# Kernel tuning notes

Measured on AMD Instinct MI355X. Metric: run time of the kernel, lower is better.

The kernel has to match this reference:

```python
import jax, jax.numpy as jnp
import numpy as np

N = 100000
E = 1600000
IN_FEATS = 256
HID = 128


def _graph_conv(x, W, b, src, dst, n_nodes):
    # DGL GraphConv with norm='both':
    #   out = D_in^{-1/2} * A * (D_out^{-1/2} * x @ W) + b
    ones = jnp.ones(src.shape[0], dtype=x.dtype)
    deg_out = jax.ops.segment_sum(ones, src, num_segments=n_nodes)
    deg_in = jax.ops.segment_sum(ones, dst, num_segments=n_nodes)
    norm_src = jnp.maximum(deg_out, 1.0) ** -0.5  # [N]
    norm_dst = jnp.maximum(deg_in, 1.0) ** -0.5   # [N]
    h = (x * norm_src[:, None]) @ W               # [N, HID]
    msg = h[src]                                  # [E, HID] gather
    agg = jax.ops.segment_sum(msg, dst, num_segments=n_nodes)  # [N, HID] scatter-add
    return agg * norm_dst[:, None] + b


def setup_inputs() -> dict:
    key = jax.random.key(0)
    ks = jax.random.split(key, 12)
    x = jax.random.normal(ks[0], (N, IN_FEATS), dtype=jnp.float32)
    src0 = jax.random.randint(ks[1], (E,), 0, N, dtype=jnp.int32)
    dst0 = jax.random.randint(ks[2], (E,), 0, N, dtype=jnp.int32)
    src1 = jax.random.randint(ks[3], (E,), 0, N, dtype=jnp.int32)
    dst1 = jax.random.randint(ks[4], (E,), 0, N, dtype=jnp.int32)
    s_e = 1.0 / np.sqrt(IN_FEATS)
    s_h = 1.0 / np.sqrt(HID)
    We = jax.random.uniform(ks[5], (IN_FEATS, HID), jnp.float32, -s_e, s_e)
    be = jax.random.uniform(ks[6], (HID,), jnp.float32, -s_e, s_e)
    W1 = jax.random.uniform(ks[7], (HID, HID), jnp.float32, -s_h, s_h)
    b1 = jnp.zeros((HID,), jnp.float32)
    W2 = jax.random.uniform(ks[8], (HID, HID), jnp.float32, -s_h, s_h)
    b2 = jnp.zeros((HID,), jnp.float32)
    return {"x": x, "We": We, "be": be, "W1": W1, "b1": b1, "W2": W2, "b2": b2,
            "src0": src0, "dst0": dst0, "src1": src1, "dst1": dst1}


def reference(x, We, be, W1, b1, W2, b2, src0, dst0, src1, dst1):
    n = x.shape[0]
    h = x @ We + be                                   # embed
    h = jax.nn.relu(_graph_conv(h, W1, b1, src0, dst0, n))
    h = jax.nn.relu(_graph_conv(h, W2, b2, src1, dst1, n))
    return h
```

## Files before the change

kernel.cpp:

```cpp
#include <hip/hip_runtime.h>

#define HID 128
#define NBUCK 512
#define BSHIFT 8
#define NB 512
#define M4 (4 * NBUCK * NB)
#define STAGE_CAP 8192

typedef __attribute__((ext_vector_type(8))) short bf16x8;
typedef __attribute__((ext_vector_type(4))) float f32x4;

__device__ __forceinline__ unsigned short f2bf(float f) {
    union { float f; unsigned u; } v; v.f = f;
    unsigned r = v.u + 0x7fff + ((v.u >> 16) & 1);
    return (unsigned short)(r >> 16);
}
__device__ __forceinline__ float bf2f(unsigned short b) {
    union { float f; unsigned u; } v; v.u = ((unsigned)b) << 16;
    return v.f;
}

__global__ __launch_bounds__(256) void bucket_count_all(
    const int* __restrict__ k0, const int* __restrict__ k1,
    const int* __restrict__ k2, const int* __restrict__ k3,
    int* __restrict__ counts, int E, int chunk) {
    __shared__ int h[4][NBUCK];
    int tid = threadIdx.x;
    #pragma unroll
    for (int j = 0; j < 8; ++j) ((int*)h)[tid + j * 256] = 0;
    __syncthreads();
    int base = blockIdx.x * chunk;
    int end = min(base + chunk, E);
    const int* keys[4] = {k0, k1, k2, k3};
    #pragma unroll
    for (int p = 0; p < 4; ++p) {
        const int* kp = keys[p];
        for (int i = base + tid; i < end; i += 256)
            atomicAdd(&h[p][kp[i] >> BSHIFT], 1);
    }
    __syncthreads();
    #pragma unroll
    for (int p = 0; p < 4; ++p) {
        counts[((p << 9) + tid) * NB + blockIdx.x] = h[p][tid];
        counts[((p << 9) + tid + 256) * NB + blockIdx.x] = h[p][tid + 256];
    }
}

__global__ __launch_bounds__(256) void scan_a(int* __restrict__ data, int* __restrict__ partials, int m) {
    __shared__ int sdata[256];
    int base = blockIdx.x * 1024;
    int tid = threadIdx.x;
    int v[4]; int s = 0;
    #pragma unroll
    for (int i = 0; i < 4; ++i) { int idx = base + tid * 4 + i; v[i] = (idx < m) ? data[idx] : 0; s += v[i]; }
    sdata[tid] = s; __syncthreads();
    for (int off = 1; off < 256; off <<= 1) {
        int t = (tid >= off) ? sdata[tid - off] : 0; __syncthreads();
        sdata[tid] += t; __syncthreads();
    }
    int excl = sdata[tid] - s;
    if (tid == 255) partials[blockIdx.x] = sdata[255];
    int run = excl;
    #pragma unroll
    for (int i = 0; i < 4; ++i) { int idx = base + tid * 4 + i; if (idx < m) data[idx] = run; run += v[i]; }
}

__global__ __launch_bounds__(1024) void scan_b(int* __restrict__ partials, int nb) {
    __shared__ int sdata[1024];
    int tid = threadIdx.x;
    int v = (tid < nb) ? partials[tid] : 0;
    sdata[tid] = v; __syncthreads();
    for (int off = 1; off < 1024; off <<= 1) {
        int t = (tid >= off) ? sdata[tid - off] : 0; __syncthreads();
        sdata[tid] += t; __syncthreads();
    }
    if (tid < nb) partials[tid] = sdata[tid] - v;
}

__global__ __launch_bounds__(256) void scan_c(int* __restrict__ data, const int* __restrict__ partials, int m) {
    int i = blockIdx.x * 256 + threadIdx.x;
    if (i < m) data[i] += partials[i >> 10];
}

__global__ __launch_bounds__(256) void bucket_scatter_all(
    const int* __restrict__ k0, const int* __restrict__ k1,
    const int* __restrict__ k2, const int* __restrict__ k3,
    const int* __restrict__ pay0, const int* __restrict__ pay1,
    const int* __restrict__ scanned, unsigned* __restrict__ bucketed,
    int E, int chunk) {
    __shared__ unsigned cur[4][NBUCK];
    int tid = threadIdx.x;
    int blk = blockIdx.x;
    #pragma unroll
    for (int p = 0; p < 4; ++p) {
        cur[p][tid]       = (unsigned)scanned[((p << 9) + tid) * NB + blk];
        cur[p][tid + 256] = (unsigned)scanned[((p << 9) + tid + 256) * NB + blk];
    }
    __syncthreads();
    int base = blk * chunk;
    int end = min(base + chunk, E);
    const int* keys[4] = {k0, k1, k2, k3};
    const int* pays[4] = {pay0, pay1, nullptr, nullptr};
    #pragma unroll
    for (int p = 0; p < 4; ++p) {
        const int* kp = keys[p];
        const int* pp = pays[p];
        for (int i = base + tid; i < end; i += 256) {
            int k = kp[i];
            int b = k >> BSHIFT;
            unsigned pay = pp ? (unsigned)pp[i] : 0u;
            unsigned pos = atomicAdd(&cur[p][b], 1u);
            bucketed[pos] = ((unsigned)(k & 255) << 17) | pay;
        }
    }
}

__global__ __launch_bounds__(256) void bucket_finalize(
    unsigned* __restrict__ bucketed, const int* __restrict__ scanned,
    int* __restrict__ rowptr0, int* __restrict__ rowptr1,
    int* __restrict__ dout0, int* __restrict__ dout1, int n, int E) {
    __shared__ unsigned stage[STAGE_CAP];
    __shared__ int cnt[256];
    __shared__ int sd[256];
    __shared__ int excl[256];
    __shared__ int cur[256];
    int tid = threadIdx.x;
    int g = blockIdx.x;
    int p = g >> 9;
    int b = g & 511;
    int start = scanned[g * NB];
    int end = (g == 4 * NBUCK - 1) ? 4 * E : scanned[(g + 1) * NB];
    if (end - start > STAGE_CAP) end = start + STAGE_CAP;
    int len = end - start;
    int node0 = b << BSHIFT;

    cnt[tid] = 0;
    __syncthreads();
    if (p < 2) {
        for (int i = tid; i < len; i += 256) {
            unsigned v = bucketed[start + i];
            stage[i] = v;
            atomicAdd(&cnt[v >> 17], 1);
        }
    } else {
        for (int i = tid; i < len; i += 256)
            atomicAdd(&cnt[bucketed[start + i] >> 17], 1);
    }
    __syncthreads();

    if (p >= 2) {
        int* dout = (p == 2) ? dout0 : dout1;
        int node = node0 + tid;
        if (node < n) dout[node] = cnt[tid];
        return;
    }

    int v = cnt[tid];
    sd[tid] = v;
    __syncthreads();
    for (int off = 1; off < 256; off <<= 1) {
        int t = (tid >= off) ? sd[tid - off] : 0; __syncthreads();
        sd[tid] += t; __syncthreads();
    }
    excl[tid] = sd[tid] - v;
    cur[tid] = 0;
    __syncthreads();

    int startLocal = start - p * E;
    int* rp = (p == 0) ? rowptr0 : rowptr1;
    int node = node0 + tid;
    if (node < n) rp[node] = startLocal + excl[tid];
    if (b == NBUCK - 1 && tid == 0) rp[n] = E;

    int* csr = (int*)bucketed + p * E;
    for (int i = tid; i < len; i += 256) {
        unsigned w = stage[i];
        int nl = (int)(w >> 17);
        int pos = startLocal + excl[nl] + atomicAdd(&cur[nl], 1);
        csr[pos] = (int)(w & 0x1FFFFu);
    }
}

__device__ __forceinline__ size_t bswz_idx(int k, int col) {
    int s = k >> 5, lh = (k >> 3) & 3, j = k & 7;
    int c = col >> 4, lc = col & 15;
    return ((((size_t)s * 8 + c) * 64 + (lh * 16 + lc)) * 8 + j);
}

__global__ __launch_bounds__(256) void weight_fuse(
    const float* __restrict__ We, const float* __restrict__ be,
    const float* __restrict__ W1,
    unsigned short* __restrict__ B1h, unsigned short* __restrict__ B1l,
    float* __restrict__ cv) {
    __shared__ float w1[128][128];
    int tid = threadIdx.x;
    #pragma unroll
    for (int it = 0; it < 16; ++it) {
        int s = tid + it * 256;
        int r = s >> 5, c4 = (s & 31) << 2;
        *(float4*)&w1[r][c4] = *(const float4*)&W1[r * 128 + c4];
    }
    __syncthreads();
    int j = tid & 127;
    int half = tid >> 7;
    if (blockIdx.x == 128) {
        if (half) return;
        float sum = 0.f;
        for (int k = 0; k < 128; ++k) sum += be[k] * w1[k][j];
        cv[j] = sum;
        return;
    }
    int i = blockIdx.x * 2 + half;
    const float* arow = &We[i * 128];
    float sum = 0.f;
    for (int k = 0; k < 128; ++k) sum += arow[k] * w1[k][j];
    unsigned short h = f2bf(sum);
    unsigned short l = f2bf(sum - bf2f(h));
    size_t o = bswz_idx(i, j);
    B1h[o] = h; B1l[o] = l;
}

__global__ __launch_bounds__(256) void swizzle_split(
    const float* __restrict__ W, unsigned short* __restrict__ Bh,
    unsigned short* __restrict__ Bl, int K) {
    int idx = blockIdx.x * 256 + threadIdx.x;
    if (idx >= K * 128) return;
    int k = idx >> 7, col = idx & 127;
    float v = W[idx];
    unsigned short h = f2bf(v);
    unsigned short l = f2bf(v - bf2f(h));
    size_t o = bswz_idx(k, col);
    Bh[o] = h; Bl[o] = l;
}

template <int K, bool AFP32>
__global__ __launch_bounds__(256) void gemm_rowmajor(
    const void* __restrict__ X_,
    const unsigned short* __restrict__ Bh, const unsigned short* __restrict__ Bl,
    const float* __restrict__ cvec, const int* __restrict__ degs,
    unsigned short* __restrict__ T, int n) {
    const int tid = threadIdx.x;
    const int wave = tid >> 6;
    const int lane = tid & 63;
    const int lr = lane & 15;
    const int lk = lane >> 4;
    const int row0 = blockIdx.x * 128 + wave * 32;

    f32x4 acc[2][8];
    #pragma unroll
    for (int rt = 0; rt < 2; ++rt)
        #pragma unroll
        for (int c = 0; c < 8; ++c) acc[rt][c] = (f32x4)0.f;

    const int r0 = row0 + lr;
    const int r1 = row0 + 16 + lr;
    const bool v0 = r0 < n, v1 = r1 < n;
    const bf16x8* pBh = (const bf16x8*)Bh;
    const bf16x8* pBl = (const bf16x8*)Bl;

    for (int s = 0; s < K / 32; ++s) {
        bf16x8 ah0 = (bf16x8)0, ah1 = (bf16x8)0, al0 = (bf16x8)0, al1 = (bf16x8)0;
        if (AFP32) {
            const float* px0 = (const float*)X_ + (size_t)r0 * K + lk * 8 + s * 32;
            const float* px1 = (const float*)X_ + (size_t)r1 * K + lk * 8 + s * 32;
            float a0[8], a1[8];
            #pragma unroll
            for (int j = 0; j < 8; ++j) { a0[j] = 0.f; a1[j] = 0.f; }
            if (v0) { *(float4*)&a0[0] = *(const float4*)px0; *(float4*)&a0[4] = *(const float4*)(px0 + 4); }
            if (v1) { *(float4*)&a1[0] = *(const float4*)px1; *(float4*)&a1[4] = *(const float4*)(px1 + 4); }
            #pragma unroll
            for (int j = 0; j < 8; ++j) {
                unsigned short h0 = f2bf(a0[j]);
                ah0[j] = (short)h0;
                al0[j] = (short)f2bf(a0[j] - bf2f(h0));
                unsigned short h1 = f2bf(a1[j]);
                ah1[j] = (short)h1;
                al1[j] = (short)f2bf(a1[j] - bf2f(h1));
            }
        } else {
            const unsigned short* ph0 = (const unsigned short*)X_ + (size_t)r0 * K + lk * 8 + s * 32;
            const unsigned short* ph1 = (const unsigned short*)X_ + (size_t)r1 * K + lk * 8 + s * 32;
            if (v0) ah0 = *(const bf16x8*)ph0;
            if (v1) ah1 = *(const bf16x8*)ph1;
        }
        const int fbase = s * 8 * 64 + lane;
        #pragma unroll
        for (int c = 0; c < 8; ++c) {
            bf16x8 bh = pBh[fbase + c * 64];
            bf16x8 bl = pBl[fbase + c * 64];
            acc[0][c] = __builtin_amdgcn_mfma_f32_16x16x32_bf16(ah0, bh, acc[0][c], 0, 0, 0);
            acc[0][c] = __builtin_amdgcn_mfma_f32_16x16x32_bf16(ah0, bl, acc[0][c], 0, 0, 0);
            acc[1][c] = __builtin_amdgcn_mfma_f32_16x16x32_bf16(ah1, bh, acc[1][c], 0, 0, 0);
            acc[1][c] = __builtin_amdgcn_mfma_f32_16x16x32_bf16(ah1, bl, acc[1][c], 0, 0, 0);
            if (AFP32) {
                acc[0][c] = __builtin_amdgcn_mfma_f32_16x16x32_bf16(al0, bh, acc[0][c], 0, 0, 0);
                acc[1][c] = __builtin_amdgcn_mfma_f32_16x16x32_bf16(al1, bh, acc[1][c], 0, 0, 0);
            }
        }
    }

    #pragma unroll
    for (int rt = 0; rt < 2; ++rt) {
        #pragma unroll
        for (int r = 0; r < 4; ++r) {
            int grow = row0 + rt * 16 + lk * 4 + r;
            if (grow >= n) continue;
            float norm = rsqrtf(fmaxf((float)degs[grow], 1.0f));
            #pragma unroll
            for (int c = 0; c < 8; ++c) {
                float v = acc[rt][c][r];
                if (cvec) v += cvec[c * 16 + lr];
                T[(size_t)grow * 128 + c * 16 + lr] = f2bf(v * norm);
            }
        }
    }
}

template <bool OUT_BF16>
__global__ __launch_bounds__(256) void aggregate(
    const unsigned short* __restrict__ T, const int* __restrict__ rowptr,
    const int* __restrict__ csr, const float* __restrict__ bias,
    void* __restrict__ out_, int n) {
    const int wave = threadIdx.x >> 6;
    const int lane = threadIdx.x & 63;
    const int half = lane >> 5;
    const int l32 = lane & 31;
    const int node = blockIdx.x * 4 + wave;
    if (node >= n) return;
    const int beg = rowptr[node], end = rowptr[node + 1];
    float a0 = 0.f, a1 = 0.f, a2 = 0.f, a3 = 0.f;
    int e = beg;
    for (; e + 15 < end; e += 16) {
        int sidx[8];
        #pragma unroll
        for (int j = 0; j < 8; ++j) sidx[j] = csr[e + j * 2 + half];
        #pragma unroll
        for (int j = 0; j < 8; ++j) {
            uint2 u = *(const uint2*)&T[(size_t)sidx[j] * 128 + l32 * 4];
            a0 += __uint_as_float(u.x << 16);
            a1 += __uint_as_float(u.x & 0xffff0000u);
            a2 += __uint_as_float(u.y << 16);
            a3 += __uint_as_float(u.y & 0xffff0000u);
        }
    }
    for (; e + 1 < end; e += 2) {
        int sidx = csr[e + half];
        uint2 u = *(const uint2*)&T[(size_t)sidx * 128 + l32 * 4];
        a0 += __uint_as_float(u.x << 16);
        a1 += __uint_as_float(u.x & 0xffff0000u);
        a2 += __uint_as_float(u.y << 16);
        a3 += __uint_as_float(u.y & 0xffff0000u);
    }
    if (e < end && half == 0) {
        int sidx = csr[e];
        uint2 u = *(const uint2*)&T[(size_t)sidx * 128 + l32 * 4];
        a0 += __uint_as_float(u.x << 16);
        a1 += __uint_as_float(u.x & 0xffff0000u);
        a2 += __uint_as_float(u.y << 16);
        a3 += __uint_as_float(u.y & 0xffff0000u);
    }
    a0 += __shfl_xor(a0, 32);
    a1 += __shfl_xor(a1, 32);
    a2 += __shfl_xor(a2, 32);
    a3 += __shfl_xor(a3, 32);
    if (half == 0) {
        float norm = rsqrtf(fmaxf((float)(end - beg), 1.0f));
        float4 bv = *(const float4*)&bias[l32 * 4];
        float o0 = fmaxf(a0 * norm + bv.x, 0.f);
        float o1 = fmaxf(a1 * norm + bv.y, 0.f);
        float o2 = fmaxf(a2 * norm + bv.z, 0.f);
        float o3 = fmaxf(a3 * norm + bv.w, 0.f);
        if (OUT_BF16) {
            unsigned w0 = (unsigned)f2bf(o0) | ((unsigned)f2bf(o1) << 16);
            unsigned w1 = (unsigned)f2bf(o2) | ((unsigned)f2bf(o3) << 16);
            uint2* dst = (uint2*)((unsigned short*)out_ + (size_t)node * 128 + l32 * 4);
            *dst = make_uint2(w0, w1);
        } else {
            float4* dst = (float4*)((float*)out_ + (size_t)node * 128 + l32 * 4);
            *dst = make_float4(o0, o1, o2, o3);
        }
    }
}

extern "C" void kernel_launch(void* const* d_in, const int* in_sizes, int n_in,
                              void* d_out, int out_size, void* d_ws, size_t ws_size,
                              hipStream_t stream) {
    const float* x   = (const float*)d_in[0];
    const float* We  = (const float*)d_in[1];
    const float* be  = (const float*)d_in[2];
    const float* W1  = (const float*)d_in[3];
    const float* b1  = (const float*)d_in[4];
    const float* W2  = (const float*)d_in[5];
    const float* b2  = (const float*)d_in[6];
    const int* src0  = (const int*)d_in[7];
    const int* dst0  = (const int*)d_in[8];
    const int* src1  = (const int*)d_in[9];
    const int* dst1  = (const int*)d_in[10];
    float* out = (float*)d_out;

    const int n = in_sizes[0] / 256;
    const int E = in_sizes[7];
    const int chunk = (E + NB - 1) / NB;

    char* p = (char*)d_ws;
    auto carve = [&](size_t bytes) -> void* {
        void* r = (void*)p;
        p += (bytes + 511) & ~(size_t)511;
        return r;
    };
    unsigned short* t        = (unsigned short*)carve((size_t)n * HID * 2);
    unsigned short* h1       = (unsigned short*)carve((size_t)n * HID * 2);
    unsigned*       bucketed = (unsigned*)carve((size_t)4 * E * 4);
    int*            counts   = (int*)carve((size_t)M4 * 4);
    int*            partials = (int*)carve(1024 * 4);
    int*            rowptr0  = (int*)carve(((size_t)n + 1) * 4);
    int*            rowptr1  = (int*)carve(((size_t)n + 1) * 4);
    int*            dout0    = (int*)carve((size_t)n * 4);
    int*            dout1    = (int*)carve((size_t)n * 4);
    unsigned short* B1h      = (unsigned short*)carve(256 * HID * 2);
    unsigned short* B1l      = (unsigned short*)carve(256 * HID * 2);
    unsigned short* B2h      = (unsigned short*)carve(128 * HID * 2);
    unsigned short* B2l      = (unsigned short*)carve(128 * HID * 2);
    float*          cv       = (float*)carve(HID * 4);

    int* csr0 = (int*)bucketed;
    int* csr1 = (int*)bucketed + E;

    const int gGemm  = (n + 127) / 128;
    const int gAggN  = (n + 3) / 4;
    const int gScanA = (M4 + 1023) / 1024;
    const int gScanC = (M4 + 255) / 256;

    bucket_count_all<<<NB, 256, 0, stream>>>(dst0, dst1, src0, src1, counts, E, chunk);
    scan_a<<<gScanA, 256, 0, stream>>>(counts, partials, M4);
    scan_b<<<1, 1024, 0, stream>>>(partials, gScanA);
    scan_c<<<gScanC, 256, 0, stream>>>(counts, partials, M4);
    bucket_scatter_all<<<NB, 256, 0, stream>>>(dst0, dst1, src0, src1, src0, src1,
                                               counts, bucketed, E, chunk);
    bucket_finalize<<<4 * NBUCK, 256, 0, stream>>>(bucketed, counts, rowptr0, rowptr1, dout0, dout1, n, E);

    weight_fuse<<<129, 256, 0, stream>>>(We, be, W1, B1h, B1l, cv);
    swizzle_split<<<(128 * 128 + 255) / 256, 256, 0, stream>>>(W2, B2h, B2l, 128);

    gemm_rowmajor<256, true><<<gGemm, 256, 0, stream>>>((const void*)x, B1h, B1l, cv, dout0, t, n);
    aggregate<true><<<gAggN, 256, 0, stream>>>(t, rowptr0, csr0, b1, (void*)h1, n);
    gemm_rowmajor<128, false><<<gGemm, 256, 0, stream>>>((const void*)h1, B2h, B2l, nullptr, dout1, t, n);
    aggregate<false><<<gAggN, 256, 0, stream>>>(t, rowptr1, csr1, b2, (void*)out, n);
}
```

Baseline: 364.2 us.

## Stage weight slabs into LDS with async double-buffered loads in GEMM

The two dense GEMM kernels now copy the pre-swizzled hi/lo bf16 weight fragments into shared memory with direct global-to-LDS loads, double-buffered across K slabs, and prefetch the next A-row slab into registers. Each wave now covers 16 rows instead of 32, so blocks handle 64 rows and the grid doubles. The aim is to hide global-load latency of the weights and the activations behind the MFMA work. In exchange, each wave gets less reuse of every weight fragment it loads, and a barrier is added per slab.

```diff
diff --git a/kernel.cpp b/kernel.cpp
--- a/kernel.cpp
+++ b/kernel.cpp
@@ -18,6 +18,12 @@
 __device__ __forceinline__ float bf2f(unsigned short b) {
     union { float f; unsigned u; } v; v.u = ((unsigned)b) << 16;
     return v.f;
+}
+
+__device__ __forceinline__ void gload_lds16(const void* g, void* l) {
+    __builtin_amdgcn_global_load_lds(
+        (const __attribute__((address_space(1))) void*)g,
+        (__attribute__((address_space(3))) void*)l, 16, 0, 0);
 }
 
 __global__ __launch_bounds__(256) void bucket_count_all(
@@ -234,84 +240,103 @@
 }
 
 template <int K, bool AFP32>
-__global__ __launch_bounds__(256) void gemm_rowmajor(
+__global__ __launch_bounds__(256) void gemm_lds(
     const void* __restrict__ X_,
     const unsigned short* __restrict__ Bh, const unsigned short* __restrict__ Bl,
     const float* __restrict__ cvec, const int* __restrict__ degs,
     unsigned short* __restrict__ T, int n) {
+    constexpr int NS = K / 32;
+    __shared__ __align__(16) char smem[2 * 16384];
     const int tid = threadIdx.x;
     const int wave = tid >> 6;
     const int lane = tid & 63;
     const int lr = lane & 15;
     const int lk = lane >> 4;
-    const int row0 = blockIdx.x * 128 + wave * 32;
-
-    f32x4 acc[2][8];
-    #pragma unroll
-    for (int rt = 0; rt < 2; ++rt)
+    const int row0 = blockIdx.x * 64 + wave * 16;
+    const int grow = row0 + lr;
+    const bool vr = grow < n;
+
+    f32x4 acc[8];
+    #pragma unroll
+    for (int c = 0; c < 8; ++c) acc[c] = (f32x4)0.f;
+
+    auto stage_slab = [&](int s, char* dst) {
         #pragma unroll
-        for (int c = 0; c < 8; ++c) acc[rt][c] = (f32x4)0.f;
-
-    const int r0 = row0 + lr;
-    const int r1 = row0 + 16 + lr;
-    const bool v0 = r0 < n, v1 = r1 < n;
-    const bf16x8* pBh = (const bf16x8*)Bh;
-    const bf16x8* pBl = (const bf16x8*)Bl;
-
-    for (int s = 0; s < K / 32; ++s) {
-        bf16x8 ah0 = (bf16x8)0, ah1 = (bf16x8)0, al0 = (bf16x8)0, al1 = (bf16x8)0;
+        for (int it = 0; it < 4; ++it) {
+            int u = tid + it * 256;
+            int f = u >> 6;
+            int c = f >> 1, plane = f & 1;
+            const unsigned short* srcArr = plane ? Bl : Bh;
+            const char* g = (const char*)srcArr +
+                ((size_t)(s * 512 + c * 64 + (u & 63)) * 16);
+            gload_lds16(g, dst + u * 16);
+        }
+    };
+
+    stage_slab(0, smem);
+
+    const float* pxf = AFP32 ? (const float*)X_ + (size_t)grow * K + lk * 8 : nullptr;
+    const unsigned short* pxb = AFP32 ? nullptr : (const unsigned short*)X_ + (size_t)grow * K + lk * 8;
+    float4 a0 = make_float4(0.f, 0.f, 0.f, 0.f), a1 = a0;
+    bf16x8 ab = (bf16x8)0;
+    if (AFP32) {
+        if (vr) { a0 = *(const float4*)pxf; a1 = *(const float4*)(pxf + 4); }
+    } else {
+        if (vr) ab = *(const bf16x8*)pxb;
+    }
+
+    #pragma unroll
+    for (int s = 0; s < NS; ++s) {
+        __syncthreads();
+        if (s + 1 < NS) stage_slab(s + 1, smem + ((s + 1) & 1) * 16384);
+
+        float4 n0 = make_float4(0.f, 0.f, 0.f, 0.f), n1 = n0;
+        bf16x8 nb = (bf16x8)0;
+        if (s + 1 < NS && vr) {
+            if (AFP32) {
+                n0 = *(const float4*)(pxf + (s + 1) * 32);
+                n1 = *(const float4*)(pxf + (s + 1) * 32 + 4);
+            } else {
+                nb = *(const bf16x8*)(pxb + (s + 1) * 32);
+            }
+        }
+
+        bf16x8 ah, al;
         if (AFP32) {
-            const float* px0 = (const float*)X_ + (size_t)r0 * K + lk * 8 + s * 32;
-            const float* px1 = (const float*)X_ + (size_t)r1 * K + lk * 8 + s * 32;
-            float a0[8], a1[8];
-            #pragma unroll
-            for (int j = 0; j < 8; ++j) { a0[j] = 0.f; a1[j] = 0.f; }
-            if (v0) { *(float4*)&a0[0] = *(const float4*)px0; *(float4*)&a0[4] = *(const float4*)(px0 + 4); }
-            if (v1) { *(float4*)&a1[0] = *(const float4*)px1; *(float4*)&a1[4] = *(const float4*)(px1 + 4); }
+            float av[8] = {a0.x, a0.y, a0.z, a0.w, a1.x, a1.y, a1.z, a1.w};
             #pragma unroll
             for (int j = 0; j < 8; ++j) {
-                unsigned short h0 = f2bf(a0[j]);
-                ah0[j] = (short)h0;
-                al0[j] = (short)f2bf(a0[j] - bf2f(h0));
-                unsigned short h1 = f2bf(a1[j]);
-                ah1[j] = (short)h1;
-                al1[j] = (short)f2bf(a1[j] - bf2f(h1));
+                unsigned short h = f2bf(av[j]);
+                ah[j] = (short)h;
+                al[j] = (short)f2bf(av[j] - bf2f(h));
             }
         } else {
-            const unsigned short* ph0 = (const unsigned short*)X_ + (size_t)r0 * K + lk * 8 + s * 32;
-            const unsigned short* ph1 = (const unsigned short*)X_ + (size_t)r1 * K + lk * 8 + s * 32;
-            if (v0) ah0 = *(const bf16x8*)ph0;
-            if (v1) ah1 = *(const bf16x8*)ph1;
-        }
-        const int fbase = s * 8 * 64 + lane;
+            ah = ab;
+        }
+
+        const char* base = smem + (s & 1) * 16384 + lane * 16;
         #pragma unroll
         for (int c = 0; c < 8; ++c) {
-            bf16x8 bh = pBh[fbase + c * 64];
-            bf16x8 bl = pBl[fbase + c * 64];
-            acc[0][c] = __builtin_amdgcn_mfma_f32_16x16x32_bf16(ah0, bh, acc[0][c], 0, 0, 0);
-            acc[0][c] = __builtin_amdgcn_mfma_f32_16x16x32_bf16(ah0, bl, acc[0][c], 0, 0, 0);
-            acc[1][c] = __builtin_amdgcn_mfma_f32_16x16x32_bf16(ah1, bh, acc[1][c], 0, 0, 0);
-            acc[1][c] = __builtin_amdgcn_mfma_f32_16x16x32_bf16(ah1, bl, acc[1][c], 0, 0, 0);
-            if (AFP32) {
-                acc[0][c] = __builtin_amdgcn_mfma_f32_16x16x32_bf16(al0, bh, acc[0][c], 0, 0, 0);
-                acc[1][c] = __builtin_amdgcn_mfma_f32_16x16x32_bf16(al1, bh, acc[1][c], 0, 0, 0);
-            }
-        }
-    }
-
-    #pragma unroll
-    for (int rt = 0; rt < 2; ++rt) {
+            bf16x8 bh = *(const bf16x8*)(base + (c * 2) * 1024);
+            bf16x8 bl = *(const bf16x8*)(base + (c * 2 + 1) * 1024);
+            acc[c] = __builtin_amdgcn_mfma_f32_16x16x32_bf16(ah, bh, acc[c], 0, 0, 0);
+            acc[c] = __builtin_amdgcn_mfma_f32_16x16x32_bf16(ah, bl, acc[c], 0, 0, 0);
+            if (AFP32)
+                acc[c] = __builtin_amdgcn_mfma_f32_16x16x32_bf16(al, bh, acc[c], 0, 0, 0);
+        }
+        a0 = n0; a1 = n1; ab = nb;
+    }
+
+    #pragma unroll
+    for (int r = 0; r < 4; ++r) {
+        int orow = row0 + lk * 4 + r;
+        if (orow >= n) continue;
+        float norm = rsqrtf(fmaxf((float)degs[orow], 1.0f));
         #pragma unroll
-        for (int r = 0; r < 4; ++r) {
-            int grow = row0 + rt * 16 + lk * 4 + r;
-            if (grow >= n) continue;
-            float norm = rsqrtf(fmaxf((float)degs[grow], 1.0f));
-            #pragma unroll
-            for (int c = 0; c < 8; ++c) {
-                float v = acc[rt][c][r];
-                if (cvec) v += cvec[c * 16 + lr];
-                T[(size_t)grow * 128 + c * 16 + lr] = f2bf(v * norm);
-            }
+        for (int c = 0; c < 8; ++c) {
+            float v = acc[c][r];
+            if (cvec) v += cvec[c * 16 + lr];
+            T[(size_t)orow * 128 + c * 16 + lr] = f2bf(v * norm);
         }
     }
 }
@@ -426,7 +451,7 @@
     int* csr0 = (int*)bucketed;
     int* csr1 = (int*)bucketed + E;
 
-    const int gGemm  = (n + 127) / 128;
+    const int gGemm  = (n + 63) / 64;
     const int gAggN  = (n + 3) / 4;
     const int gScanA = (M4 + 1023) / 1024;
     const int gScanC = (M4 + 255) / 256;
@@ -442,8 +467,8 @@
     weight_fuse<<<129, 256, 0, stream>>>(We, be, W1, B1h, B1l, cv);
     swizzle_split<<<(128 * 128 + 255) / 256, 256, 0, stream>>>(W2, B2h, B2l, 128);
 
-    gemm_rowmajor<256, true><<<gGemm, 256, 0, stream>>>((const void*)x, B1h, B1l, cv, dout0, t, n);
+    gemm_lds<256, true><<<gGemm, 256, 0, stream>>>((const void*)x, B1h, B1l, cv, dout0, t, n);
     aggregate<true><<<gAggN, 256, 0, stream>>>(t, rowptr0, csr0, b1, (void*)h1, n);
-    gemm_rowmajor<128, false><<<gGemm, 256, 0, stream>>>((const void*)h1, B2h, B2l, nullptr, dout1, t, n);
+    gemm_lds<128, false><<<gGemm, 256, 0, stream>>>((const void*)h1, B2h, B2l, nullptr, dout1, t, n);
     aggregate<false><<<gAggN, 256, 0, stream>>>(t, rowptr1, csr1, b2, (void*)out, n);
 }
```

Measured after the change: 326.9 us. -10.2%, faster.
